# Kernel tuning notes

Measured on AMD Instinct MI355X. Metric: run time of the kernel, lower is better.

Reference implementation:

```python
import jax, jax.numpy as jnp
import numpy as np

D_IN = 2048
D_OUT = 2048
NUM_HEADS = 16
HEAD_DIM = D_OUT // NUM_HEADS
LATENT = 256
B, S = 2, 2048


def setup_inputs() -> dict:
    key = jax.random.key(0)
    ks = jax.random.split(key, 7)
    s = lambda fan_in: 1.0 / np.sqrt(fan_in)
    return {
        "x": jax.random.normal(ks[0], (B, S, D_IN), dtype=jnp.float32),
        "W_query": jax.random.normal(ks[1], (D_IN, D_OUT), dtype=jnp.float32) * s(D_IN),
        "W_DKV": jax.random.normal(ks[2], (D_IN, LATENT), dtype=jnp.float32) * s(D_IN),
        "W_UK": jax.random.normal(ks[3], (LATENT, D_OUT), dtype=jnp.float32) * s(LATENT),
        "W_UV": jax.random.normal(ks[4], (LATENT, D_OUT), dtype=jnp.float32) * s(LATENT),
        "W_out": jax.random.normal(ks[5], (D_OUT, D_OUT), dtype=jnp.float32) * s(D_OUT),
        "b_out": jax.random.normal(ks[6], (D_OUT,), dtype=jnp.float32) * 0.01,
    }


def reference(x, W_query, W_DKV, W_UK, W_UV, W_out, b_out):
    b, n, _ = x.shape
    # projections
    q = x @ W_query                      # [b, n, d_out]
    latent = x @ W_DKV                   # [b, n, latent]
    k = latent @ W_UK                    # [b, n, d_out]
    v = latent @ W_UV                    # [b, n, d_out]
    # split heads -> [b, h, n, hd]
    to_heads = lambda t: t.reshape(b, n, NUM_HEADS, HEAD_DIM).transpose(0, 2, 1, 3)
    q, k, v = to_heads(q), to_heads(k), to_heads(v)
    scores = jnp.einsum("bhqd,bhkd->bhqk", q, k)
    # causal mask: q_pos < k_pos masked to -inf (applied BEFORE scaling, as in source)
    qpos = jnp.arange(n)[:, None]
    kpos = jnp.arange(n)[None, :]
    scores = jnp.where(qpos < kpos, -jnp.inf, scores)
    attn = jax.nn.softmax(scores / np.sqrt(HEAD_DIM), axis=-1)
    ctx = jnp.einsum("bhqk,bhkd->bhqd", attn, v)   # [b, h, n, hd]
    ctx = ctx.transpose(0, 2, 1, 3).reshape(b, n, D_OUT)
    return ctx @ W_out + b_out
```

## Files before the change

### kernel.cpp

```cpp
#include <hip/hip_runtime.h>

#define DIN 2048
#define DOUT 2048
#define NHEADS 16
#define HDIM 128
#define LATENT 256
#define BB 2
#define SS 2048
#define MTOT (BB*SS)
#define QLD (DOUT + LATENT)
#define KLD (2*DOUT)

using bf16 = __bf16;
using bf16x8 = __attribute__((ext_vector_type(8))) __bf16;
using f32x4 = __attribute__((ext_vector_type(4))) float;

__device__ __forceinline__ void gload16(const bf16* g, bf16* l) {
    __builtin_amdgcn_global_load_lds(
        (const __attribute__((address_space(1))) void*)g,
        (__attribute__((address_space(3))) void*)l, 16, 0, 0);
}

__global__ void cast_f32_bf16(const float* __restrict__ in, bf16* __restrict__ out, int n) {
    int i = (blockIdx.x * blockDim.x + threadIdx.x) * 8;
    if (i >= n) return;
    float4 a = *(const float4*)(in + i);
    float4 b = *(const float4*)(in + i + 4);
    bf16x8 o;
    o[0] = (bf16)a.x; o[1] = (bf16)a.y; o[2] = (bf16)a.z; o[3] = (bf16)a.w;
    o[4] = (bf16)b.x; o[5] = (bf16)b.y; o[6] = (bf16)b.z; o[7] = (bf16)b.w;
    *(bf16x8*)(out + i) = o;
}

__global__ void transpose_cast(const float* __restrict__ W, bf16* __restrict__ WT, int R, int C) {
    __shared__ float tile[32][33];
    int c0 = blockIdx.x * 32, r0 = blockIdx.y * 32;
    int tx = threadIdx.x & 31, ty = threadIdx.x >> 5;
    #pragma unroll
    for (int i = ty; i < 32; i += 8)
        tile[i][tx] = W[(size_t)(r0 + i) * C + c0 + tx];
    __syncthreads();
    #pragma unroll
    for (int i = ty; i < 32; i += 8)
        WT[(size_t)(c0 + i) * R + r0 + tx] = (bf16)tile[tx][i];
}

__global__ void transpose_v(const bf16* __restrict__ v, bf16* __restrict__ vT) {
    int bh = blockIdx.z;
    int s0 = blockIdx.x * 32, d0 = blockIdx.y * 32;
    __shared__ bf16 t[32][33];
    int tx = threadIdx.x & 31, ty = threadIdx.x >> 5;
    int b = bh >> 4, h = bh & 15;
    #pragma unroll
    for (int i = ty; i < 32; i += 8)
        t[i][tx] = v[(size_t)(b * SS + s0 + i) * KLD + h * HDIM + d0 + tx];
    __syncthreads();
    #pragma unroll
    for (int i = ty; i < 32; i += 8)
        vT[((size_t)bh * HDIM + d0 + i) * SS + s0 + tx] = t[tx][i];
}

template<bool OUT_F32, bool BIAS>
__global__ __launch_bounds__(256) void gemm_bt(const bf16* __restrict__ A,
        const bf16* __restrict__ BT, void* __restrict__ Cp,
        const float* __restrict__ bias, const int Kdim, const int Ald,
        const int Ndim, const int Cld) {
    const int nwg = gridDim.x * gridDim.y;
    int orig = blockIdx.y * gridDim.x + blockIdx.x;
    int swz = (orig & 7) * (nwg >> 3) + (orig >> 3);
    const int n0 = (swz % gridDim.x) * 128, m0 = (swz / gridDim.x) * 128;

    const int tid = threadIdx.x, wave = tid >> 6, lane = tid & 63;
    const int wm = wave >> 1, wn = wave & 1;
    const int lr = lane & 15, lg = lane >> 4;
    __shared__ __align__(16) bf16 As[128][32];
    __shared__ __align__(16) bf16 Bs[128][32];
    f32x4 acc[4][4];
    #pragma unroll
    for (int i = 0; i < 4; ++i)
        #pragma unroll
        for (int j = 0; j < 4; ++j) acc[i][j] = (f32x4){0.f, 0.f, 0.f, 0.f};

    const int sr = lane >> 2;
    const int sc = (lane & 3) * 8;
    const bf16* ga = A  + (size_t)(m0 + wave * 16 + sr) * Ald + sc;
    const bf16* gb = BT + (size_t)(n0 + wave * 16 + sr) * Kdim + sc;
    const size_t strideA64 = (size_t)64 * Ald;
    const size_t strideB64 = (size_t)64 * Kdim;
    bf16* lAd = &As[wave * 16][0];
    bf16* lBd = &Bs[wave * 16][0];

    for (int k0 = 0; k0 < Kdim; k0 += 32) {
        gload16(ga,             lAd);
        gload16(ga + strideA64, lAd + 64 * 32);
        gload16(gb,             lBd);
        gload16(gb + strideB64, lBd + 64 * 32);
        ga += 32; gb += 32;
        __syncthreads();
        bf16x8 af[4], bfr[4];
        #pragma unroll
        for (int i = 0; i < 4; ++i)
            af[i] = *(const bf16x8*)&As[wm * 64 + i * 16 + lr][lg * 8];
        #pragma unroll
        for (int j = 0; j < 4; ++j)
            bfr[j] = *(const bf16x8*)&Bs[wn * 64 + j * 16 + lr][lg * 8];
        #pragma unroll
        for (int i = 0; i < 4; ++i)
            #pragma unroll
            for (int j = 0; j < 4; ++j)
                acc[i][j] = __builtin_amdgcn_mfma_f32_16x16x32_bf16(af[i], bfr[j], acc[i][j], 0, 0, 0);
        __syncthreads();
    }
    #pragma unroll
    for (int i = 0; i < 4; ++i)
        #pragma unroll
        for (int j = 0; j < 4; ++j) {
            const int r0 = m0 + wm * 64 + i * 16 + lg * 4;
            const int c = n0 + wn * 64 + j * 16 + lr;
            #pragma unroll
            for (int r2 = 0; r2 < 4; ++r2) {
                float v = acc[i][j][r2];
                if (BIAS) v += bias[c];
                if (OUT_F32) ((float*)Cp)[(size_t)(r0 + r2) * Cld + c] = v;
                else         ((bf16*)Cp)[(size_t)(r0 + r2) * Cld + c] = (bf16)v;
            }
        }
}

__global__ __launch_bounds__(256, 4) void attn_kernel(const bf16* __restrict__ q,
        const bf16* __restrict__ k, const bf16* __restrict__ vT, bf16* __restrict__ ctx) {
    int orig = blockIdx.y * 16 + blockIdx.x;
    int swz = (orig & 7) * 64 + (orig >> 3);
    const int bx = swz & 15, bh = swz >> 4;
    const int b = bh >> 4, h = bh & 15;
    const int tid = threadIdx.x, wave = tid >> 6, lane = tid & 63;
    const int lr = lane & 15, lg = lane >> 4;

    __shared__ __align__(16) char KsB[2 * 16384];
    __shared__ __align__(16) char VsB[2 * 16384];
    __shared__ __align__(16) char PsB[64 * 128];

    int krow[4], kcolE[4];
    #pragma unroll
    for (int c = 0; c < 4; ++c) {
        krow[c] = wave * 16 + c * 4 + (lane >> 4);
        kcolE[c] = ((((lane & 15) * 16) ^ ((krow[c] & 7) << 4)) >> 1);
    }
    const int vrow0 = wave * 32 + (lane >> 3);
    const int vcolE = ((((lane & 7) * 16) ^ ((lane >> 3) << 4)) >> 1);

    const bf16* kbaseP = k  + (size_t)b * SS * KLD + h * HDIM;
    const bf16* vbaseP = vT + (size_t)bh * HDIM * SS;

    const float C = 0.12752602f;

    int cur = 0;
    for (int half = 0; half < 2; ++half) {
        const int qt = half ? (31 - bx) : bx;
        const int q0 = qt * 64;

        bf16x8 qf[4];
        const bf16* qbase = q + ((size_t)(b * SS + q0 + wave * 16 + lr)) * QLD + h * HDIM;
        #pragma unroll
        for (int d = 0; d < 4; ++d) qf[d] = *(const bf16x8*)(qbase + d * 32 + lg * 8);

        f32x4 o[8];
        #pragma unroll
        for (int i = 0; i < 8; ++i) o[i] = (f32x4){0.f, 0.f, 0.f, 0.f};
        float m_i[4], l_i[4];
        #pragma unroll
        for (int r = 0; r < 4; ++r) { m_i[r] = -3.0e38f; l_i[r] = 0.f; }

        const int nkt = qt + 1;

        {
            bf16* dK = (bf16*)(KsB + cur * 16384 + wave * 4096);
            bf16* dV = (bf16*)(VsB + cur * 16384 + wave * 4096);
            #pragma unroll
            for (int c = 0; c < 4; ++c) {
                gload16(kbaseP + (size_t)krow[c] * KLD + kcolE[c], dK + c * 512);
                gload16(vbaseP + (size_t)(vrow0 + c * 8) * SS + vcolE, dV + c * 512);
            }
        }
        __syncthreads();

        for (int kt = 0; kt < nkt; ++kt) {
            const int kbase = kt * 64;
            if (kt + 1 < nkt) {
                const int kb2 = kbase + 64;
                bf16* dK = (bf16*)(KsB + (cur ^ 1) * 16384 + wave * 4096);
                bf16* dV = (bf16*)(VsB + (cur ^ 1) * 16384 + wave * 4096);
                #pragma unroll
                for (int c = 0; c < 4; ++c) {
                    gload16(kbaseP + (size_t)(kb2 + krow[c]) * KLD + kcolE[c], dK + c * 512);
                    gload16(vbaseP + (size_t)(vrow0 + c * 8) * SS + kb2 + vcolE, dV + c * 512);
                }
            }
            const char* KB = KsB + cur * 16384;
            const char* VB = VsB + cur * 16384;

            f32x4 sacc[4];
            #pragma unroll
            for (int nf = 0; nf < 4; ++nf) sacc[nf] = (f32x4){0.f, 0.f, 0.f, 0.f};
            __builtin_amdgcn_s_setprio(1);
            #pragma unroll
            for (int nf = 0; nf < 4; ++nf)
                #pragma unroll
                for (int d = 0; d < 4; ++d) {
                    int row = nf * 16 + lr;
                    bf16x8 kf = *(const bf16x8*)(KB + ((row * 256 + d * 64 + lg * 16) ^ ((row & 7) << 4)));
                    sacc[nf] = __builtin_amdgcn_mfma_f32_16x16x32_bf16(qf[d], kf, sacc[nf], 0, 0, 0);
                }
            __builtin_amdgcn_s_setprio(0);

            float sv[4][4];
            const bool maskt = (kbase + 63 > q0);
            #pragma unroll
            for (int nf = 0; nf < 4; ++nf)
                #pragma unroll
                for (int r = 0; r < 4; ++r) {
                    float s = sacc[nf][r];
                    if (maskt) {
                        int qr = q0 + wave * 16 + lg * 4 + r;
                        int kc = kbase + nf * 16 + lr;
                        if (qr < kc) s = -3.0e38f;
                    }
                    sv[nf][r] = s;
                }
            float corr[4];
            #pragma unroll
            for (int r = 0; r < 4; ++r) {
                float v = fmaxf(fmaxf(sv[0][r], sv[1][r]), fmaxf(sv[2][r], sv[3][r]));
                #pragma unroll
                for (int off = 1; off < 16; off <<= 1) v = fmaxf(v, __shfl_xor(v, off));
                float mnew = fmaxf(m_i[r], v);
                corr[r] = __builtin_amdgcn_exp2f((m_i[r] - mnew) * C);
                m_i[r] = mnew;
            }
            float rsum[4] = {0.f, 0.f, 0.f, 0.f};
            #pragma unroll
            for (int nf = 0; nf < 4; ++nf)
                #pragma unroll
                for (int r = 0; r < 4; ++r) {
                    float p = __builtin_amdgcn_exp2f((sv[nf][r] - m_i[r]) * C);
                    rsum[r] += p;
                    int prow = wave * 16 + lg * 4 + r;
                    *(bf16*)(PsB + ((prow * 128 + (nf * 16 + lr) * 2) ^ ((prow & 7) << 4))) = (bf16)p;
                }
            #pragma unroll
            for (int r = 0; r < 4; ++r) {
                float v = rsum[r];
                #pragma unroll
                for (int off = 1; off < 16; off <<= 1) v += __shfl_xor(v, off);
                l_i[r] = l_i[r] * corr[r] + v;
            }
            #pragma unroll
            for (int df = 0; df < 8; ++df)
                #pragma unroll
                for (int r = 0; r < 4; ++r) o[df][r] *= corr[r];

            __builtin_amdgcn_s_setprio(1);
            #pragma unroll
            for (int ks = 0; ks < 2; ++ks) {
                int prow = wave * 16 + lr;
                bf16x8 pf = *(const bf16x8*)(PsB + ((prow * 128 + ks * 64 + lg * 16) ^ ((prow & 7) << 4)));
                #pragma unroll
                for (int df = 0; df < 8; ++df) {
                    int vr2 = df * 16 + lr;
                    bf16x8 vf = *(const bf16x8*)(VB + ((vr2 * 128 + ks * 64 + lg * 16) ^ ((vr2 & 7) << 4)));
                    o[df] = __builtin_amdgcn_mfma_f32_16x16x32_bf16(pf, vf, o[df], 0, 0, 0);
                }
            }
            __builtin_amdgcn_s_setprio(0);
            __syncthreads();
            cur ^= 1;
        }

        #pragma unroll
        for (int r = 0; r < 4; ++r) {
            float inv = 1.0f / l_i[r];
            #pragma unroll
            for (int df = 0; df < 8; ++df) {
                int rrow = q0 + wave * 16 + lg * 4 + r;
                int col = h * HDIM + df * 16 + lr;
                ctx[(size_t)(b * SS + rrow) * DOUT + col] = (bf16)(o[df][r] * inv);
            }
        }
    }
}

extern "C" void kernel_launch(void* const* d_in, const int* in_sizes, int n_in,
                              void* d_out, int out_size, void* d_ws, size_t ws_size,
                              hipStream_t stream) {
    const float* x    = (const float*)d_in[0];
    const float* Wq   = (const float*)d_in[1];
    const float* Wdkv = (const float*)d_in[2];
    const float* Wuk  = (const float*)d_in[3];
    const float* Wuv  = (const float*)d_in[4];
    const float* Wout = (const float*)d_in[5];
    const float* bout = (const float*)d_in[6];

    char* ws = (char*)d_ws;
    size_t off = 0;
    auto alloc = [&](size_t bytes) { char* p = ws + off; off = (off + bytes + 255) & ~255ULL; return p; };
    bf16* xb    = (bf16*)alloc((size_t)MTOT * DIN * 2);
    bf16* WqT   = (bf16*)alloc((size_t)DOUT * DIN * 2);
    bf16* WdkvT = (bf16*)alloc((size_t)LATENT * DIN * 2);
    bf16* WukT  = (bf16*)alloc((size_t)DOUT * LATENT * 2);
    bf16* WuvT  = (bf16*)alloc((size_t)DOUT * LATENT * 2);
    bf16* WoutT = (bf16*)alloc((size_t)DOUT * DOUT * 2);
    bf16* qlat  = (bf16*)alloc((size_t)MTOT * QLD * 2);
    bf16* kvb   = (bf16*)alloc((size_t)MTOT * KLD * 2);
    bf16* vT    = (bf16*)alloc((size_t)BB * NHEADS * HDIM * SS * 2);
    bf16* ctx   = (bf16*)alloc((size_t)MTOT * DOUT * 2);

    cast_f32_bf16<<<(MTOT * DIN) / 8 / 256, 256, 0, stream>>>(x, xb, MTOT * DIN);
    transpose_cast<<<dim3(DOUT / 32, DIN / 32), 256, 0, stream>>>(Wq, WqT, DIN, DOUT);
    transpose_cast<<<dim3(LATENT / 32, DIN / 32), 256, 0, stream>>>(Wdkv, WdkvT, DIN, LATENT);
    transpose_cast<<<dim3(DOUT / 32, LATENT / 32), 256, 0, stream>>>(Wuk, WukT, LATENT, DOUT);
    transpose_cast<<<dim3(DOUT / 32, LATENT / 32), 256, 0, stream>>>(Wuv, WuvT, LATENT, DOUT);
    transpose_cast<<<dim3(DOUT / 32, DOUT / 32), 256, 0, stream>>>(Wout, WoutT, DOUT, DOUT);

    gemm_bt<false, false><<<dim3(QLD / 128, MTOT / 128), 256, 0, stream>>>(
        xb, WqT, qlat, nullptr, DIN, DIN, QLD, QLD);
    gemm_bt<false, false><<<dim3(KLD / 128, MTOT / 128), 256, 0, stream>>>(
        qlat + DOUT, WukT, kvb, nullptr, LATENT, QLD, KLD, KLD);

    transpose_v<<<dim3(SS / 32, HDIM / 32, BB * NHEADS), 256, 0, stream>>>(kvb + DOUT, vT);

    attn_kernel<<<dim3(16, BB * NHEADS), 256, 0, stream>>>(qlat, kvb, vT, ctx);

    gemm_bt<true, true><<<dim3(DOUT / 128, MTOT / 128), 256, 0, stream>>>(
        ctx, WoutT, d_out, bout, DOUT, DOUT, DOUT, DOUT);
}
```

Baseline: 379.9 us.

## Use lazy softmax rescaling, single-buffer K/V tiles, and merge weight transposes

The attention kernel now rescales the running max and accumulators only when some row's new tile max exceeds the old one by a threshold, uses one FMA per exponent, and defers the row-sum shuffle reduction to the end. K/V staging drops from double to single buffering, so loads are issued and waited on each iteration but LDS use shrinks, which may allow more resident blocks. Weight transpose launches are merged pairwise through a z-indexed kernel. The threshold rescaling lets exponents grow up to 2^8 before correction, and losing the prefetch exposes global-load latency.

```diff
diff --git a/kernel.cpp b/kernel.cpp
--- a/kernel.cpp
+++ b/kernel.cpp
@@ -45,6 +45,23 @@
         WT[(size_t)(c0 + i) * R + r0 + tx] = (bf16)tile[tx][i];
 }
 
+__global__ void transpose_cast2(const float* __restrict__ W0, bf16* __restrict__ T0,
+                                const float* __restrict__ W1, bf16* __restrict__ T1,
+                                int R, int C) {
+    const float* W = blockIdx.z ? W1 : W0;
+    bf16* WT = blockIdx.z ? T1 : T0;
+    __shared__ float tile[32][33];
+    int c0 = blockIdx.x * 32, r0 = blockIdx.y * 32;
+    int tx = threadIdx.x & 31, ty = threadIdx.x >> 5;
+    #pragma unroll
+    for (int i = ty; i < 32; i += 8)
+        tile[i][tx] = W[(size_t)(r0 + i) * C + c0 + tx];
+    __syncthreads();
+    #pragma unroll
+    for (int i = ty; i < 32; i += 8)
+        WT[(size_t)(c0 + i) * R + r0 + tx] = (bf16)tile[tx][i];
+}
+
 __global__ void transpose_v(const bf16* __restrict__ v, bf16* __restrict__ vT) {
     int bh = blockIdx.z;
     int s0 = blockIdx.x * 32, d0 = blockIdx.y * 32;
@@ -136,9 +153,9 @@
     const int tid = threadIdx.x, wave = tid >> 6, lane = tid & 63;
     const int lr = lane & 15, lg = lane >> 4;
 
-    __shared__ __align__(16) char KsB[2 * 16384];
-    __shared__ __align__(16) char VsB[2 * 16384];
-    __shared__ __align__(16) char PsB[64 * 128];
+    __shared__ __align__(16) char KsB[16384];
+    __shared__ __align__(16) char VsB[16384];
+    __shared__ __align__(16) char PsB[8192];
 
     int krow[4], kcolE[4];
     #pragma unroll
@@ -147,14 +164,13 @@
         kcolE[c] = ((((lane & 15) * 16) ^ ((krow[c] & 7) << 4)) >> 1);
     }
     const int vrow0 = wave * 32 + (lane >> 3);
-    const int vcolE = ((((lane & 7) * 16) ^ ((lane >> 3) << 4)) >> 1);
+    const int vcolE = ((((lane & 7) * 16) ^ (((lane >> 3) & 7) << 4)) >> 1);
 
     const bf16* kbaseP = k  + (size_t)b * SS * KLD + h * HDIM;
     const bf16* vbaseP = vT + (size_t)bh * HDIM * SS;
 
-    const float C = 0.12752602f;
-
-    int cur = 0;
+    const float C = 0.12751743f;
+
     for (int half = 0; half < 2; ++half) {
         const int qt = half ? (31 - bx) : bx;
         const int q0 = qt * 64;
@@ -167,37 +183,23 @@
         f32x4 o[8];
         #pragma unroll
         for (int i = 0; i < 8; ++i) o[i] = (f32x4){0.f, 0.f, 0.f, 0.f};
-        float m_i[4], l_i[4];
-        #pragma unroll
-        for (int r = 0; r < 4; ++r) { m_i[r] = -3.0e38f; l_i[r] = 0.f; }
+        float m_i[4], lp[4], mC[4];
+        #pragma unroll
+        for (int r = 0; r < 4; ++r) { m_i[r] = -3.0e38f; lp[r] = 0.f; mC[r] = -3.8e37f; }
 
         const int nkt = qt + 1;
-
-        {
-            bf16* dK = (bf16*)(KsB + cur * 16384 + wave * 4096);
-            bf16* dV = (bf16*)(VsB + cur * 16384 + wave * 4096);
-            #pragma unroll
-            for (int c = 0; c < 4; ++c) {
-                gload16(kbaseP + (size_t)krow[c] * KLD + kcolE[c], dK + c * 512);
-                gload16(vbaseP + (size_t)(vrow0 + c * 8) * SS + vcolE, dV + c * 512);
-            }
-        }
-        __syncthreads();
-
         for (int kt = 0; kt < nkt; ++kt) {
             const int kbase = kt * 64;
-            if (kt + 1 < nkt) {
-                const int kb2 = kbase + 64;
-                bf16* dK = (bf16*)(KsB + (cur ^ 1) * 16384 + wave * 4096);
-                bf16* dV = (bf16*)(VsB + (cur ^ 1) * 16384 + wave * 4096);
+            {
+                bf16* dK = (bf16*)(KsB + wave * 4096);
+                bf16* dV = (bf16*)(VsB + wave * 4096);
                 #pragma unroll
                 for (int c = 0; c < 4; ++c) {
-                    gload16(kbaseP + (size_t)(kb2 + krow[c]) * KLD + kcolE[c], dK + c * 512);
-                    gload16(vbaseP + (size_t)(vrow0 + c * 8) * SS + kb2 + vcolE, dV + c * 512);
-                }
-            }
-            const char* KB = KsB + cur * 16384;
-            const char* VB = VsB + cur * 16384;
+                    gload16(kbaseP + (size_t)(kbase + krow[c]) * KLD + kcolE[c], dK + c * 512);
+                    gload16(vbaseP + (size_t)(vrow0 + c * 8) * SS + kbase + vcolE, dV + c * 512);
+                }
+            }
+            __syncthreads();
 
             f32x4 sacc[4];
             #pragma unroll
@@ -208,7 +210,7 @@
                 #pragma unroll
                 for (int d = 0; d < 4; ++d) {
                     int row = nf * 16 + lr;
-                    bf16x8 kf = *(const bf16x8*)(KB + ((row * 256 + d * 64 + lg * 16) ^ ((row & 7) << 4)));
+                    bf16x8 kf = *(const bf16x8*)(KsB + ((row * 256 + d * 64 + lg * 16) ^ ((row & 7) << 4)));
                     sacc[nf] = __builtin_amdgcn_mfma_f32_16x16x32_bf16(qf[d], kf, sacc[nf], 0, 0, 0);
                 }
             __builtin_amdgcn_s_setprio(0);
@@ -227,37 +229,37 @@
                     }
                     sv[nf][r] = s;
                 }
-            float corr[4];
+            float tmax[4];
             #pragma unroll
             for (int r = 0; r < 4; ++r) {
                 float v = fmaxf(fmaxf(sv[0][r], sv[1][r]), fmaxf(sv[2][r], sv[3][r]));
                 #pragma unroll
                 for (int off = 1; off < 16; off <<= 1) v = fmaxf(v, __shfl_xor(v, off));
-                float mnew = fmaxf(m_i[r], v);
-                corr[r] = __builtin_amdgcn_exp2f((m_i[r] - mnew) * C);
-                m_i[r] = mnew;
-            }
-            float rsum[4] = {0.f, 0.f, 0.f, 0.f};
+                tmax[r] = v;
+            }
+            bool need = false;
+            #pragma unroll
+            for (int r = 0; r < 4; ++r) need = need || ((tmax[r] - m_i[r]) * C > 8.0f);
+            if (__any(need)) {
+                #pragma unroll
+                for (int r = 0; r < 4; ++r) {
+                    float mnew = fmaxf(m_i[r], tmax[r]);
+                    float corr = __builtin_amdgcn_exp2f((m_i[r] - mnew) * C);
+                    m_i[r] = mnew; mC[r] = mnew * C;
+                    lp[r] *= corr;
+                    #pragma unroll
+                    for (int df = 0; df < 8; ++df) o[df][r] *= corr;
+                }
+            }
             #pragma unroll
             for (int nf = 0; nf < 4; ++nf)
                 #pragma unroll
                 for (int r = 0; r < 4; ++r) {
-                    float p = __builtin_amdgcn_exp2f((sv[nf][r] - m_i[r]) * C);
-                    rsum[r] += p;
+                    float p = __builtin_amdgcn_exp2f(fmaf(sv[nf][r], C, -mC[r]));
+                    lp[r] += p;
                     int prow = wave * 16 + lg * 4 + r;
                     *(bf16*)(PsB + ((prow * 128 + (nf * 16 + lr) * 2) ^ ((prow & 7) << 4))) = (bf16)p;
                 }
-            #pragma unroll
-            for (int r = 0; r < 4; ++r) {
-                float v = rsum[r];
-                #pragma unroll
-                for (int off = 1; off < 16; off <<= 1) v += __shfl_xor(v, off);
-                l_i[r] = l_i[r] * corr[r] + v;
-            }
-            #pragma unroll
-            for (int df = 0; df < 8; ++df)
-                #pragma unroll
-                for (int r = 0; r < 4; ++r) o[df][r] *= corr[r];
 
             __builtin_amdgcn_s_setprio(1);
             #pragma unroll
@@ -267,18 +269,20 @@
                 #pragma unroll
                 for (int df = 0; df < 8; ++df) {
                     int vr2 = df * 16 + lr;
-                    bf16x8 vf = *(const bf16x8*)(VB + ((vr2 * 128 + ks * 64 + lg * 16) ^ ((vr2 & 7) << 4)));
+                    bf16x8 vf = *(const bf16x8*)(VsB + ((vr2 * 128 + ks * 64 + lg * 16) ^ ((vr2 & 7) << 4)));
                     o[df] = __builtin_amdgcn_mfma_f32_16x16x32_bf16(pf, vf, o[df], 0, 0, 0);
                 }
             }
             __builtin_amdgcn_s_setprio(0);
             __syncthreads();
-            cur ^= 1;
         }
 
         #pragma unroll
         for (int r = 0; r < 4; ++r) {
-            float inv = 1.0f / l_i[r];
+            float v = lp[r];
+            #pragma unroll
+            for (int off = 1; off < 16; off <<= 1) v += __shfl_xor(v, off);
+            float inv = 1.0f / v;
             #pragma unroll
             for (int df = 0; df < 8; ++df) {
                 int rrow = q0 + wave * 16 + lg * 4 + r;
@@ -315,11 +319,9 @@
     bf16* ctx   = (bf16*)alloc((size_t)MTOT * DOUT * 2);
 
     cast_f32_bf16<<<(MTOT * DIN) / 8 / 256, 256, 0, stream>>>(x, xb, MTOT * DIN);
-    transpose_cast<<<dim3(DOUT / 32, DIN / 32), 256, 0, stream>>>(Wq, WqT, DIN, DOUT);
+    transpose_cast2<<<dim3(DOUT / 32, DIN / 32, 2), 256, 0, stream>>>(Wq, WqT, Wout, WoutT, DIN, DOUT);
+    transpose_cast2<<<dim3(DOUT / 32, LATENT / 32, 2), 256, 0, stream>>>(Wuk, WukT, Wuv, WuvT, LATENT, DOUT);
     transpose_cast<<<dim3(LATENT / 32, DIN / 32), 256, 0, stream>>>(Wdkv, WdkvT, DIN, LATENT);
-    transpose_cast<<<dim3(DOUT / 32, LATENT / 32), 256, 0, stream>>>(Wuk, WukT, LATENT, DOUT);
-    transpose_cast<<<dim3(DOUT / 32, LATENT / 32), 256, 0, stream>>>(Wuv, WuvT, LATENT, DOUT);
-    transpose_cast<<<dim3(DOUT / 32, DOUT / 32), 256, 0, stream>>>(Wout, WoutT, DOUT, DOUT);
 
     gemm_bt<false, false><<<dim3(QLD / 128, MTOT / 128), 256, 0, stream>>>(
         xb, WqT, qlat, nullptr, DIN, DIN, QLD, QLD);
```

Result: slower. 493.2 us (+29.8%).
